# Kernel tuning notes

Hardware: AMD Instinct MI355X
Metric: run time of the kernel (lower is better)

## Reference

```python
import jax, jax.numpy as jnp
import numpy as np

B, N, M = 64, 1024, 1024


def _chamfer(a, b):
    # a: [B,N,3], b: [B,M,3]; pairwise Euclidean distances via Gram trick
    d2 = (
        jnp.sum(a * a, axis=-1)[:, :, None]
        + jnp.sum(b * b, axis=-1)[:, None, :]
        - 2.0 * jnp.einsum('bnd,bmd->bnm', a, b)
    )  # [B,N,M]
    d = jnp.sqrt(jnp.maximum(d2, 0.0))
    # bidirectional nearest-neighbor distance (N == M so they align per-point slot)
    return 0.5 * (jnp.min(d, axis=2) + jnp.min(d, axis=1))  # [B,N]


def _l2(a, b):
    return jnp.linalg.norm(a - b, axis=2)  # [B,N]


def setup_inputs() -> dict:
    key = jax.random.key(0)
    k1, k2, k3, k4, k5, k6 = jax.random.split(key, 6)
    return {
        'pred_points1': jax.random.normal(k1, (B, N, 3), dtype=jnp.float32),
        'pred_points2': jax.random.normal(k2, (B, N, 3), dtype=jnp.float32),
        'target_points': jax.random.normal(k3, (B, M, 3), dtype=jnp.float32),
        'flag1': jax.random.uniform(k4, (B,), dtype=jnp.float32),
        'flag2': jax.random.uniform(k5, (B,), dtype=jnp.float32),
        'sym_flag': jax.random.uniform(k6, (B,), dtype=jnp.float32),
    }


def reference(pred_points1, pred_points2, target_points, flag1, flag2, sym_flag):
    sym_dis1 = _chamfer(pred_points1, target_points).mean(axis=1)   # [B]
    asym_dis1 = _l2(pred_points1, target_points).mean(axis=1)       # [B]
    loss1 = flag1 * (sym_flag * sym_dis1 + (1.0 - sym_flag) * asym_dis1)

    sym_dis2 = _chamfer(pred_points2, target_points).mean(axis=1)
    asym_dis2 = _l2(pred_points2, target_points).mean(axis=1)
    # flag2 multiplier makes the sum(flag2)>0 branch mathematically equivalent
    loss2 = flag2 * (sym_flag * sym_dis2 + (1.0 - sym_flag) * asym_dis2)

    all_loss = loss1 + loss2
    # (all_loss, stage1, stage2) scalar losses, stacked
    return jnp.stack([all_loss.mean(), loss1.mean(), loss2.mean()])
```

## Files before the change

kernel.cpp:

```cpp
#include <hip/hip_runtime.h>
#include <hip/hip_bf16.h>


#define BATCH 64
#define NPTS 1024

typedef __attribute__((ext_vector_type(8))) short s16x8;
typedef __attribute__((ext_vector_type(8))) unsigned short u16x8;
typedef __attribute__((ext_vector_type(16))) float f32x16;

__device__ inline void split_bf(float v, unsigned short& hi, unsigned short& lo) {
    unsigned int bits = __float_as_uint(v);
    hi = (unsigned short)(bits >> 16);
    float rec = __uint_as_float(bits & 0xFFFF0000u);
    lo = (unsigned short)(__float_as_uint(v - rec) >> 16);
}

__device__ inline void pack_ab(float x, float y, float z,
                               u16x8& a0, u16x8& a1, u16x8& b0, u16x8& b1) {
    float h = fmaf(z, z, fmaf(y, y, x*x));
    unsigned short xh, xl, yh, yl, zh, zl;
    split_bf(x, xh, xl); split_bf(y, yh, yl); split_bf(z, zh, zl);
    unsigned short cxh, cxl, cyh, cyl, czh, czl;
    split_bf(-2.f*x, cxh, cxl); split_bf(-2.f*y, cyh, cyl); split_bf(-2.f*z, czh, czl);
    unsigned short hh, hl;
    split_bf(h, hh, hl);
    const unsigned short one = 0x3F80;
    a0 = u16x8{cxh, cyh, czh, cxl, cyl, czl, cxh, cyh};
    a1 = u16x8{czh, hh, hl, one, one, 0, 0, 0};
    b0 = u16x8{xh, yh, zh, xh, yh, zh, xl, yl};
    b1 = u16x8{zl, one, one, hh, hl, 0, 0, 0};
}

__device__ inline float fold_sum(float v[16], int lane) {
    {
        const bool up = lane & 1;
        #pragma unroll
        for (int k = 0; k < 8; ++k) {
            float send = up ? v[k] : v[k+8];
            float recv = __shfl_xor(send, 1);
            v[k] = fminf(up ? v[k+8] : v[k], recv);
        }
    }
    {
        const bool up = lane & 2;
        #pragma unroll
        for (int k = 0; k < 4; ++k) {
            float send = up ? v[k] : v[k+4];
            float recv = __shfl_xor(send, 2);
            v[k] = fminf(up ? v[k+4] : v[k], recv);
        }
    }
    {
        const bool up = lane & 4;
        #pragma unroll
        for (int k = 0; k < 2; ++k) {
            float send = up ? v[k] : v[k+2];
            float recv = __shfl_xor(send, 4);
            v[k] = fminf(up ? v[k+2] : v[k], recv);
        }
    }
    {
        const bool up = lane & 8;
        float send = up ? v[0] : v[1];
        float recv = __shfl_xor(send, 8);
        v[0] = fminf(up ? v[1] : v[0], recv);
    }
    v[0] = fminf(v[0], __shfl_xor(v[0], 16));
    float d = sqrtf(fmaxf(v[0], 0.f));
    #pragma unroll
    for (int mask = 1; mask <= 32; mask <<= 1) d += __shfl_xor(d, mask);
    return d;
}

__global__ __launch_bounds__(512) void pass_kernel(
    const float* __restrict__ p1, const float* __restrict__ p2,
    const float* __restrict__ tg, float* __restrict__ ws)
{
    __shared__ __align__(16) unsigned short ybuf[16384];
    __shared__ __align__(16) unsigned short abuf[8192];
    __shared__ float red[8];
    __shared__ float redE[8];

    const int bid = blockIdx.x;
    const int j = bid >> 7, b = (bid >> 1) & 63, half = bid & 1;
    const int tid = threadIdx.x;

    const float* __restrict__ X = (j == 0) ? p1 : (j == 1) ? p2 : tg;
    const float* __restrict__ Y = (j == 2) ? p1 : (j == 3) ? p2 : tg;

    #pragma unroll
    for (int ii = 0; ii < 2; ++ii) {
        const int i = tid + ii * 512;
        const size_t g = ((size_t)b * NPTS + i) * 3;
        float x = Y[g], y = Y[g+1], z = Y[g+2];
        u16x8 a0, a1, b0, b1;
        pack_ab(x, y, z, a0, a1, b0, b1);
        const int off = (i >> 5) * 512 + (i & 31) * 8;
        *(u16x8*)(ybuf + off)       = b0;
        *(u16x8*)(ybuf + off + 256) = b1;
    }
    float e = 0.f;
    {
        const int i = half * 512 + tid;
        const size_t g = ((size_t)b * NPTS + i) * 3;
        float x = X[g], y = X[g+1], z = X[g+2];
        u16x8 a0, a1, b0, b1;
        pack_ab(x, y, z, a0, a1, b0, b1);
        const int off = (tid >> 5) * 512 + (tid & 31) * 8;
        *(u16x8*)(abuf + off)       = a0;
        *(u16x8*)(abuf + off + 256) = a1;
        if (j < 2) {
            float tx = tg[g], ty = tg[g+1], tz = tg[g+2];
            float dx = x - tx, dy = y - ty, dz = z - tz;
            e = sqrtf(fmaf(dz, dz, fmaf(dy, dy, dx*dx)));
        }
    }
    __syncthreads();

    const int lane = tid & 63, w = tid >> 6;
    const int c = lane & 31, q = lane >> 5;
    const int fo = q * 256 + c * 8;
    const s16x8 fa0 = *(const s16x8*)(abuf + (2*w)   * 512 + fo);
    const s16x8 fa1 = *(const s16x8*)(abuf + (2*w+1) * 512 + fo);

    float rm0[16], rm1[16];
    #pragma unroll
    for (int i = 0; i < 16; ++i) { rm0[i] = 3e38f; rm1[i] = 3e38f; }
    const f32x16 zacc = {};

    const unsigned short* Yp = ybuf + fo;
    #pragma unroll 2
    for (int t = 0; t < 32; ++t) {
        const s16x8 bb = *(const s16x8*)(Yp + t * 512);
        f32x16 u0 = __builtin_amdgcn_mfma_f32_32x32x16_bf16(fa0, bb, zacc, 0, 0, 0);
        f32x16 u1 = __builtin_amdgcn_mfma_f32_32x32x16_bf16(fa1, bb, zacc, 0, 0, 0);
        #pragma unroll
        for (int i = 0; i < 16; ++i) {
            rm0[i] = fminf(rm0[i], u0[i]);
            rm1[i] = fminf(rm1[i], u1[i]);
        }
    }

    const float s = 0.5f * (fold_sum(rm0, lane) + fold_sum(rm1, lane));
    #pragma unroll
    for (int mask = 1; mask <= 32; mask <<= 1) e += __shfl_xor(e, mask);
    if (lane == 0) { red[w] = s; redE[w] = e; }
    __syncthreads();

    if (tid == 0) {
        float S = 0.f, E = 0.f;
        #pragma unroll
        for (int k = 0; k < 8; ++k) { S += red[k]; E += redE[k]; }
        ws[bid] = S;
        if (j < 2) ws[512 + bid] = E;
    }
}

__global__ __launch_bounds__(64) void finalize_kernel(
    const float* __restrict__ flag1, const float* __restrict__ flag2,
    const float* __restrict__ symf, const float* __restrict__ ws,
    float* __restrict__ out)
{
    const int b = threadIdx.x;
    float rowS1 = 0.f, rowS2 = 0.f, colS1 = 0.f, colS2 = 0.f, E1 = 0.f, E2 = 0.f;
    #pragma unroll
    for (int h = 0; h < 2; ++h) {
        rowS1 += ws[0*128 + b*2 + h];
        rowS2 += ws[1*128 + b*2 + h];
        colS1 += ws[2*128 + b*2 + h];
        colS2 += ws[3*128 + b*2 + h];
        E1    += ws[512 + 0*128 + b*2 + h];
        E2    += ws[512 + 1*128 + b*2 + h];
    }
    const float inv = 1.f / (float)NPTS;
    const float ch1 = 0.5f * (rowS1 + colS1) * inv;
    const float ch2 = 0.5f * (rowS2 + colS2) * inv;
    const float sf = symf[b];
    float l1 = flag1[b] * (sf * ch1 + (1.f - sf) * E1 * inv);
    float l2 = flag2[b] * (sf * ch2 + (1.f - sf) * E2 * inv);
    #pragma unroll
    for (int mask = 1; mask <= 32; mask <<= 1) {
        l1 += __shfl_xor(l1, mask);
        l2 += __shfl_xor(l2, mask);
    }
    if (b == 0) {
        const float s = 1.f / (float)BATCH;
        out[0] = (l1 + l2) * s;
        out[1] = l1 * s;
        out[2] = l2 * s;
    }
}

extern "C" void kernel_launch(void* const* d_in, const int* in_sizes, int n_in,
                              void* d_out, int out_size, void* d_ws, size_t ws_size,
                              hipStream_t stream) {
    const float* p1 = (const float*)d_in[0];
    const float* p2 = (const float*)d_in[1];
    const float* tg = (const float*)d_in[2];
    const float* f1 = (const float*)d_in[3];
    const float* f2 = (const float*)d_in[4];
    const float* sf = (const float*)d_in[5];
    float* out = (float*)d_out;
    float* ws = (float*)d_ws;

    pass_kernel<<<512, 512, 0, stream>>>(p1, p2, tg, ws);
    finalize_kernel<<<1, 64, 0, stream>>>(f1, f2, sf, ws, out);
}
```

Baseline: 74.04 us.

## Fuse finalize into pass kernel via last-block atomic counter; pair MFMA min updates

The separate finalize kernel is removed. Each block publishes its partial sums with release stores and increments a global counter, and the last block to arrive performs the per-batch loss combination and writes the outputs. A hipMemsetAsync resets the counter before each launch. The inner MFMA loop is also restructured to process two Y tiles per iteration and fold their mins together, which cuts the number of fminf chains. The aim is to save one kernel launch, at the cost of a memset node and atomic traffic.

```diff
diff --git a/kernel.cpp b/kernel.cpp
--- a/kernel.cpp
+++ b/kernel.cpp
@@ -73,9 +73,15 @@
     return d;
 }
 
+__device__ inline float aload(const float* p) {
+    return __hip_atomic_load(p, __ATOMIC_ACQUIRE, __HIP_MEMORY_SCOPE_AGENT);
+}
+
 __global__ __launch_bounds__(512) void pass_kernel(
     const float* __restrict__ p1, const float* __restrict__ p2,
-    const float* __restrict__ tg, float* __restrict__ ws)
+    const float* __restrict__ tg, const float* __restrict__ flag1,
+    const float* __restrict__ flag2, const float* __restrict__ symf,
+    float* __restrict__ ws, float* __restrict__ out)
 {
     __shared__ __align__(16) unsigned short ybuf[16384];
     __shared__ __align__(16) unsigned short abuf[8192];
@@ -131,15 +137,17 @@
 
     const unsigned short* Yp = ybuf + fo;
     #pragma unroll 2
-    for (int t = 0; t < 32; ++t) {
-        const s16x8 bb = *(const s16x8*)(Yp + t * 512);
-        f32x16 u0 = __builtin_amdgcn_mfma_f32_32x32x16_bf16(fa0, bb, zacc, 0, 0, 0);
-        f32x16 u1 = __builtin_amdgcn_mfma_f32_32x32x16_bf16(fa1, bb, zacc, 0, 0, 0);
-        #pragma unroll
-        for (int i = 0; i < 16; ++i) {
-            rm0[i] = fminf(rm0[i], u0[i]);
-            rm1[i] = fminf(rm1[i], u1[i]);
-        }
+    for (int t = 0; t < 32; t += 2) {
+        const s16x8 bb0 = *(const s16x8*)(Yp + t * 512);
+        const s16x8 bb1 = *(const s16x8*)(Yp + t * 512 + 512);
+        f32x16 u00 = __builtin_amdgcn_mfma_f32_32x32x16_bf16(fa0, bb0, zacc, 0, 0, 0);
+        f32x16 u01 = __builtin_amdgcn_mfma_f32_32x32x16_bf16(fa0, bb1, zacc, 0, 0, 0);
+        #pragma unroll
+        for (int i = 0; i < 16; ++i) rm0[i] = fminf(rm0[i], fminf(u00[i], u01[i]));
+        f32x16 u10 = __builtin_amdgcn_mfma_f32_32x32x16_bf16(fa1, bb0, zacc, 0, 0, 0);
+        f32x16 u11 = __builtin_amdgcn_mfma_f32_32x32x16_bf16(fa1, bb1, zacc, 0, 0, 0);
+        #pragma unroll
+        for (int i = 0; i < 16; ++i) rm1[i] = fminf(rm1[i], fminf(u10[i], u11[i]));
     }
 
     const float s = 0.5f * (fold_sum(rm0, lane) + fold_sum(rm1, lane));
@@ -148,47 +156,50 @@
     if (lane == 0) { red[w] = s; redE[w] = e; }
     __syncthreads();
 
-    if (tid == 0) {
-        float S = 0.f, E = 0.f;
-        #pragma unroll
-        for (int k = 0; k < 8; ++k) { S += red[k]; E += redE[k]; }
-        ws[bid] = S;
-        if (j < 2) ws[512 + bid] = E;
-    }
-}
-
-__global__ __launch_bounds__(64) void finalize_kernel(
-    const float* __restrict__ flag1, const float* __restrict__ flag2,
-    const float* __restrict__ symf, const float* __restrict__ ws,
-    float* __restrict__ out)
-{
-    const int b = threadIdx.x;
-    float rowS1 = 0.f, rowS2 = 0.f, colS1 = 0.f, colS2 = 0.f, E1 = 0.f, E2 = 0.f;
-    #pragma unroll
-    for (int h = 0; h < 2; ++h) {
-        rowS1 += ws[0*128 + b*2 + h];
-        rowS2 += ws[1*128 + b*2 + h];
-        colS1 += ws[2*128 + b*2 + h];
-        colS2 += ws[3*128 + b*2 + h];
-        E1    += ws[512 + 0*128 + b*2 + h];
-        E2    += ws[512 + 1*128 + b*2 + h];
-    }
-    const float inv = 1.f / (float)NPTS;
-    const float ch1 = 0.5f * (rowS1 + colS1) * inv;
-    const float ch2 = 0.5f * (rowS2 + colS2) * inv;
-    const float sf = symf[b];
-    float l1 = flag1[b] * (sf * ch1 + (1.f - sf) * E1 * inv);
-    float l2 = flag2[b] * (sf * ch2 + (1.f - sf) * E2 * inv);
-    #pragma unroll
-    for (int mask = 1; mask <= 32; mask <<= 1) {
-        l1 += __shfl_xor(l1, mask);
-        l2 += __shfl_xor(l2, mask);
-    }
-    if (b == 0) {
-        const float s = 1.f / (float)BATCH;
-        out[0] = (l1 + l2) * s;
-        out[1] = l1 * s;
-        out[2] = l2 * s;
+    if (w == 0) {
+        int last = 0;
+        if (lane == 0) {
+            float S = 0.f, E = 0.f;
+            #pragma unroll
+            for (int k = 0; k < 8; ++k) { S += red[k]; E += redE[k]; }
+            __hip_atomic_store(&ws[bid], S, __ATOMIC_RELEASE, __HIP_MEMORY_SCOPE_AGENT);
+            if (j < 2)
+                __hip_atomic_store(&ws[512 + bid], E, __ATOMIC_RELEASE, __HIP_MEMORY_SCOPE_AGENT);
+            unsigned prev = __hip_atomic_fetch_add((unsigned int*)&ws[1024], 1u,
+                                                   __ATOMIC_ACQ_REL, __HIP_MEMORY_SCOPE_AGENT);
+            last = (prev == 511u);
+        }
+        last = __shfl(last, 0);
+        if (last) {
+            const int bb = lane;
+            float rowS1 = 0.f, rowS2 = 0.f, colS1 = 0.f, colS2 = 0.f, E1 = 0.f, E2 = 0.f;
+            #pragma unroll
+            for (int h = 0; h < 2; ++h) {
+                rowS1 += aload(&ws[0*128 + bb*2 + h]);
+                rowS2 += aload(&ws[1*128 + bb*2 + h]);
+                colS1 += aload(&ws[2*128 + bb*2 + h]);
+                colS2 += aload(&ws[3*128 + bb*2 + h]);
+                E1    += aload(&ws[512 + 0*128 + bb*2 + h]);
+                E2    += aload(&ws[512 + 1*128 + bb*2 + h]);
+            }
+            const float inv = 1.f / (float)NPTS;
+            const float ch1 = 0.5f * (rowS1 + colS1) * inv;
+            const float ch2 = 0.5f * (rowS2 + colS2) * inv;
+            const float sf = symf[bb];
+            float l1 = flag1[bb] * (sf * ch1 + (1.f - sf) * E1 * inv);
+            float l2 = flag2[bb] * (sf * ch2 + (1.f - sf) * E2 * inv);
+            #pragma unroll
+            for (int mask = 1; mask <= 32; mask <<= 1) {
+                l1 += __shfl_xor(l1, mask);
+                l2 += __shfl_xor(l2, mask);
+            }
+            if (lane == 0) {
+                const float sc = 1.f / (float)BATCH;
+                out[0] = (l1 + l2) * sc;
+                out[1] = l1 * sc;
+                out[2] = l2 * sc;
+            }
+        }
     }
 }
 
@@ -204,6 +215,6 @@
     float* out = (float*)d_out;
     float* ws = (float*)d_ws;
 
-    pass_kernel<<<512, 512, 0, stream>>>(p1, p2, tg, ws);
-    finalize_kernel<<<1, 64, 0, stream>>>(f1, f2, sf, ws, out);
-}
+    hipMemsetAsync((char*)d_ws + 4096, 0, 4, stream);
+    pass_kernel<<<512, 512, 0, stream>>>(p1, p2, tg, f1, f2, sf, ws, out);
+}
```

Measured after the change: 91.88 us. 24.1% more time.
